# Performance work log

Hardware: AMD Instinct MI355X
Metric: run time of the kernel (lower is better)

The kernel has to match this reference:

```python
import jax, jax.numpy as jnp
import numpy as np

B, C, H, W = 2, 256, 64, 64
NUM_HEADS = 4
DIM_HEAD_QK = 64
DIM_HEAD_V = 64  # dim_out // num_heads
DIM_OUT_QK = NUM_HEADS * DIM_HEAD_QK  # 256
DIM_OUT_V = NUM_HEADS * DIM_HEAD_V    # 256
SCALE = DIM_HEAD_QK ** -0.5


def rel_logits_1d(q, rel_k, permute):
    # q: (Bh, Hq, Wq, d), rel_k: (2*Wq-1, d)
    Bh, Hq, Wq, d = q.shape
    R = 2 * Wq - 1
    x = jnp.einsum('bhwd,rd->bhwr', q, rel_k)              # (Bh, Hq, Wq, R)
    x = x.reshape(-1, Wq, R)
    x_pad = jnp.pad(x, ((0, 0), (0, 0), (0, 1))).reshape(x.shape[0], -1)
    x_pad = jnp.pad(x_pad, ((0, 0), (0, Wq - 1)))
    x_pad = x_pad.reshape(-1, Wq + 1, R)
    x = x_pad[:, :Wq, Wq - 1:]                              # (Bh*Hq, Wq, Wq)
    x = x.reshape(Bh, Hq, 1, Wq, Wq)
    x = jnp.broadcast_to(x, (Bh, Hq, Hq, Wq, Wq))
    return jnp.transpose(x, permute)


def pos_embed_rel(q, height_rel, width_rel):
    # q: (Bh, HW, d)
    Bh = q.shape[0]
    qr = q.reshape(Bh, H, W, -1)
    rel_w = rel_logits_1d(qr, width_rel, (0, 1, 3, 2, 4))   # (Bh, H, W, H, W)
    qt = jnp.transpose(qr, (0, 2, 1, 3))                    # (Bh, W, H, d)
    rel_h = rel_logits_1d(qt, height_rel, (0, 3, 1, 4, 2))  # (Bh, H, W, H, W)
    return (rel_h + rel_w).reshape(Bh, H * W, H * W)


def setup_inputs() -> dict:
    key = jax.random.key(0)
    k1, k2, k3, k4 = jax.random.split(key, 4)
    x = jax.random.normal(k1, (B, C, H, W), dtype=jnp.float32)
    qkv_w = jax.random.normal(k2, (2 * DIM_OUT_QK + DIM_OUT_V, C), dtype=jnp.float32) * (C ** -0.5)
    height_rel = jax.random.normal(k3, (2 * H - 1, DIM_HEAD_QK), dtype=jnp.float32) * SCALE
    width_rel = jax.random.normal(k4, (2 * W - 1, DIM_HEAD_QK), dtype=jnp.float32) * SCALE
    return {"x": x, "qkv_w": qkv_w, "height_rel": height_rel, "width_rel": width_rel}


def reference(x, qkv_w, height_rel, width_rel):
    # 1x1 conv == channel matmul
    qkv = jnp.einsum('bchw,oc->bohw', x, qkv_w)             # (B, 768, H, W)
    q, k, v = jnp.split(qkv, [DIM_OUT_QK, 2 * DIM_OUT_QK], axis=1)
    HW = H * W
    q = q.reshape(B * NUM_HEADS, DIM_HEAD_QK, HW).transpose(0, 2, 1)  # (Bh, HW, d)
    k = k.reshape(B * NUM_HEADS, DIM_HEAD_QK, HW)                     # (Bh, d, HW)
    v = v.reshape(B * NUM_HEADS, DIM_HEAD_V, HW).transpose(0, 2, 1)   # (Bh, HW, dv)
    attn = jnp.einsum('bnd,bdm->bnm', q, k) * SCALE + pos_embed_rel(q, height_rel, width_rel)
    attn = jax.nn.softmax(attn, axis=-1)
    out = jnp.einsum('bnm,bmd->bnd', attn, v)               # (Bh, HW, dv)
    out = out.transpose(0, 2, 1).reshape(B, DIM_OUT_V, H, W)
    return out
```

## Files before the change

### kernel.cpp

```cpp
#include <hip/hip_runtime.h>
#include <hip/hip_bf16.h>

typedef __attribute__((ext_vector_type(8))) short bf16x8;
typedef __attribute__((ext_vector_type(4))) float f32x4;

static __device__ __forceinline__ f32x4 mfma16(bf16x8 a, bf16x8 b, f32x4 c) {
    return __builtin_amdgcn_mfma_f32_16x16x32_bf16(a, b, c, 0, 0, 0);
}

#define LOG2E 1.44269504f

__global__ __launch_bounds__(256, 4) void qkv_kernel(
    const float* __restrict__ x, const float* __restrict__ w,
    __hip_bfloat16* __restrict__ qb, __hip_bfloat16* __restrict__ kb,
    __hip_bfloat16* __restrict__ vt)
{
    alignas(16) __shared__ __hip_bfloat16 sA[64 * 72];
    alignas(16) __shared__ __hip_bfloat16 sB[64 * 72];
    const int nb = blockIdx.x * 64;
    const int ob = blockIdx.y * 64;
    const int b  = blockIdx.z;
    const int tid  = threadIdx.x;
    const int lane = tid & 63;
    const int wv   = tid >> 6;
    const int quad = lane >> 4;
    const int l16  = lane & 15;

    f32x4 acc[4];
    for (int i = 0; i < 4; i++) acc[i] = (f32x4)0.f;

    for (int k0 = 0; k0 < 256; k0 += 64) {
        __syncthreads();
        {
            const int o = tid >> 2, c0 = (tid & 3) << 4;
            const float* srcw = w + (ob + o) * 256 + k0 + c0;
            union { bf16x8 v; __hip_bfloat16 h[8]; } u0, u1;
            #pragma unroll
            for (int i = 0; i < 2; i++) {
                float4 f = *(const float4*)(srcw + i * 4);
                u0.h[4*i+0] = __float2bfloat16(f.x); u0.h[4*i+1] = __float2bfloat16(f.y);
                u0.h[4*i+2] = __float2bfloat16(f.z); u0.h[4*i+3] = __float2bfloat16(f.w);
            }
            #pragma unroll
            for (int i = 0; i < 2; i++) {
                float4 f = *(const float4*)(srcw + 8 + i * 4);
                u1.h[4*i+0] = __float2bfloat16(f.x); u1.h[4*i+1] = __float2bfloat16(f.y);
                u1.h[4*i+2] = __float2bfloat16(f.z); u1.h[4*i+3] = __float2bfloat16(f.w);
            }
            *(bf16x8*)&sA[o * 72 + c0]     = u0.v;
            *(bf16x8*)&sA[o * 72 + c0 + 8] = u1.v;
        }
        {
            const int c = tid >> 2, n0 = (tid & 3) << 4;
            const float* srcx = x + ((size_t)b * 256 + k0 + c) * 4096 + nb + n0;
            #pragma unroll
            for (int i = 0; i < 4; i++) {
                float4 f = *(const float4*)(srcx + i * 4);
                sB[(n0 + 4*i + 0) * 72 + c] = __float2bfloat16(f.x);
                sB[(n0 + 4*i + 1) * 72 + c] = __float2bfloat16(f.y);
                sB[(n0 + 4*i + 2) * 72 + c] = __float2bfloat16(f.z);
                sB[(n0 + 4*i + 3) * 72 + c] = __float2bfloat16(f.w);
            }
        }
        __syncthreads();
        const __hip_bfloat16* aRow = &sA[(16 * wv + l16) * 72];
        #pragma unroll
        for (int ks = 0; ks < 2; ks++) {
            bf16x8 af = *(const bf16x8*)&aRow[ks * 32 + quad * 8];
            #pragma unroll
            for (int ct = 0; ct < 4; ct++) {
                bf16x8 bfv = *(const bf16x8*)&sB[(16 * ct + l16) * 72 + ks * 32 + quad * 8];
                acc[ct] = mfma16(af, bfv, acc[ct]);
            }
        }
    }
    if (ob < 512) {
        #pragma unroll
        for (int ct = 0; ct < 4; ct++) {
            int n = nb + 16 * ct + l16;
            int o0 = ob + 16 * wv + quad * 4;
            union { short4 s; __hip_bfloat16 hh[4]; } u;
            #pragma unroll
            for (int r = 0; r < 4; r++) u.hh[r] = __float2bfloat16(acc[ct][r]);
            int oo = o0 & 255;
            int bhh = b * 4 + (oo >> 6), d = oo & 63;
            __hip_bfloat16* dst = (o0 >= 256 ? kb : qb) + ((size_t)bhh * 4096 + n) * 64 + d;
            *(short4*)dst = u.s;
        }
    } else {
        __syncthreads();
        #pragma unroll
        for (int ct = 0; ct < 4; ct++)
            #pragma unroll
            for (int r = 0; r < 4; r++)
                sA[(16 * wv + quad * 4 + r) * 72 + 16 * ct + l16] = __float2bfloat16(acc[ct][r]);
        int o2 = (ob - 512) + 16 * wv + l16;
        int bhh = b * 4 + (o2 >> 6), d = o2 & 63;
        __hip_bfloat16* dst = vt + ((size_t)bhh * 64 + d) * 4096 + nb + 16 * quad;
        const __hip_bfloat16* srcl = &sA[(16 * wv + l16) * 72 + 16 * quad];
        *(bf16x8*)dst       = *(const bf16x8*)srcl;
        *(bf16x8*)(dst + 8) = *(const bf16x8*)(srcl + 8);
    }
}

__global__ __launch_bounds__(512, 4) void attn_kernel(
    const __hip_bfloat16* __restrict__ qb, const __hip_bfloat16* __restrict__ kb,
    const __hip_bfloat16* __restrict__ vt, const float* __restrict__ hrel,
    const float* __restrict__ wrel, float* __restrict__ out)
{
    alignas(16) __shared__ __hip_bfloat16 sU[18432];
    alignas(16) __shared__ __hip_bfloat16 sRH[64 * 66];

    const int h    = blockIdx.x;
    const int bh   = blockIdx.y;
    const int tid  = threadIdx.x;
    const int lane = tid & 63;
    const int wv   = tid >> 6;
    const int qg   = wv >> 2;
    const int kg   = wv & 3;
    const int quad = lane >> 4;
    const int l16  = lane & 15;

    __hip_bfloat16* sQ   = sU;
    __hip_bfloat16* sW   = sU + 64 * 72;
    __hip_bfloat16* sHRs = sU + 192 * 72;
    __hip_bfloat16* sRWt = sU;
    __hip_bfloat16* sKb  = sU;
    __hip_bfloat16* sVb  = sU + 128 * 72;

    {
        int r = tid >> 3, d8 = (tid & 7) * 8;
        *(bf16x8*)&sQ[r * 72 + d8] =
            *(const bf16x8*)&qb[(((size_t)bh * 4096 + h * 64 + r)) * 64 + d8];
    }
    {
        int r = tid >> 2, c0 = (tid & 3) << 4;
        union { bf16x8 v; __hip_bfloat16 h8[8]; } u0, u1;
        #pragma unroll
        for (int i = 0; i < 2; i++) {
            float4 f = (r < 127) ? *(const float4*)&wrel[r * 64 + c0 + 4*i] : float4{0,0,0,0};
            u0.h8[4*i+0] = __float2bfloat16(f.x); u0.h8[4*i+1] = __float2bfloat16(f.y);
            u0.h8[4*i+2] = __float2bfloat16(f.z); u0.h8[4*i+3] = __float2bfloat16(f.w);
        }
        #pragma unroll
        for (int i = 0; i < 2; i++) {
            float4 f = (r < 127) ? *(const float4*)&wrel[r * 64 + c0 + 8 + 4*i] : float4{0,0,0,0};
            u1.h8[4*i+0] = __float2bfloat16(f.x); u1.h8[4*i+1] = __float2bfloat16(f.y);
            u1.h8[4*i+2] = __float2bfloat16(f.z); u1.h8[4*i+3] = __float2bfloat16(f.w);
        }
        *(bf16x8*)&sW[r * 72 + c0]     = u0.v;
        *(bf16x8*)&sW[r * 72 + c0 + 8] = u1.v;
    }
    {
        int r = tid >> 3, c0 = (tid & 7) * 8;
        union { bf16x8 v; __hip_bfloat16 h8[8]; } u0;
        #pragma unroll
        for (int i = 0; i < 2; i++) {
            float4 f = *(const float4*)&hrel[(63 - h + r) * 64 + c0 + 4*i];
            u0.h8[4*i+0] = __float2bfloat16(f.x); u0.h8[4*i+1] = __float2bfloat16(f.y);
            u0.h8[4*i+2] = __float2bfloat16(f.z); u0.h8[4*i+3] = __float2bfloat16(f.w);
        }
        *(bf16x8*)&sHRs[r * 72 + c0] = u0.v;
    }
    __syncthreads();

    const int g    = wv & 3;
    const int half = wv >> 2;
    const __hip_bfloat16* aRow = &sQ[(16 * g + l16) * 72];
    bf16x8 qf0 = *(const bf16x8*)&aRow[quad * 8];
    bf16x8 qf1 = *(const bf16x8*)&aRow[32 + quad * 8];
    bf16x8 qm[2][2];
    #pragma unroll
    for (int qt = 0; qt < 2; qt++) {
        const __hip_bfloat16* qr = &sQ[(qg * 32 + 16 * qt + l16) * 72];
        qm[qt][0] = *(const bf16x8*)&qr[quad * 8];
        qm[qt][1] = *(const bf16x8*)&qr[32 + quad * 8];
    }
    __syncthreads();

    {
        const int rbase = half * 64;
        #pragma unroll
        for (int ct = 0; ct < 4; ct++) {
            int rr = rbase + 16 * ct + l16;
            f32x4 a = (f32x4)0.f;
            a = mfma16(qf0, *(const bf16x8*)&sW[rr * 72 + quad * 8], a);
            a = mfma16(qf1, *(const bf16x8*)&sW[rr * 72 + 32 + quad * 8], a);
            #pragma unroll
            for (int r = 0; r < 4; r++) {
                int ww = 16 * g + quad * 4 + r;
                int wp = rr + ww - 63;
                if (wp >= 0 && wp < 64) sRWt[ww * 68 + wp] = __float2bfloat16(a[r]);
            }
        }
    }
    if (half == 0) {
        #pragma unroll
        for (int ct = 0; ct < 4; ct++) {
            f32x4 a = (f32x4)0.f;
            a = mfma16(qf0, *(const bf16x8*)&sHRs[(16 * ct + l16) * 72 + quad * 8], a);
            a = mfma16(qf1, *(const bf16x8*)&sHRs[(16 * ct + l16) * 72 + 32 + quad * 8], a);
            #pragma unroll
            for (int r = 0; r < 4; r++)
                sRH[(16 * g + quad * 4 + r) * 66 + 16 * ct + l16] = __float2bfloat16(a[r]);
        }
    }
    __syncthreads();

    union S4 { short4 s; __hip_bfloat16 h[4]; };
    S4 rwp[2][2];
    #pragma unroll
    for (int qt = 0; qt < 2; qt++)
        #pragma unroll
        for (int kt = 0; kt < 2; kt++)
            rwp[qt][kt].s = *(const short4*)&sRWt[(qg * 32 + 16 * qt + l16) * 68
                                                  + 32 * (kg & 1) + 16 * kt + 4 * quad];
    __syncthreads();

    f32x4 oacc[2][4];
    #pragma unroll
    for (int qt = 0; qt < 2; qt++)
        #pragma unroll
        for (int dt = 0; dt < 4; dt++) oacc[qt][dt] = (f32x4)0.f;
    float lsum[2] = {0.f, 0.f};

    const __hip_bfloat16* ksrc = kb + (size_t)bh * 4096 * 64;
    const __hip_bfloat16* vsrc = vt + (size_t)bh * 64 * 4096;

    const int skey = tid >> 2, sd16 = (tid & 3) * 16;
    const int svd  = tid >> 3, sq3  = tid & 7;
    const int skg  = sq3 >> 1, st   = sq3 & 1;
    __hip_bfloat16* stK = &sKb[skey * 72 + sd16];
    __hip_bfloat16* stV = &sVb[svd * 136 + skg * 32 + st * 4];
    const __hip_bfloat16* gK = ksrc + (size_t)skey * 64 + sd16;
    const __hip_bfloat16* gV = vsrc + (size_t)svd * 4096 + sq3 * 16;

    bf16x8 pk0, pk1, pv0, pv1;
    pk0 = *(const bf16x8*)(gK);
    pk1 = *(const bf16x8*)(gK + 8);
    pv0 = *(const bf16x8*)(gV);
    pv1 = *(const bf16x8*)(gV + 8);

    const __hip_bfloat16* kr0  = &sKb[(kg * 32 + l16) * 72 + quad * 8];
    const __hip_bfloat16* vrow = &sVb[l16 * 136 + kg * 32 + quad * 8];
    const __hip_bfloat16* rh0  = &sRH[(qg * 32 + l16) * 66];
    const __hip_bfloat16* rh1  = &sRH[(qg * 32 + 16 + l16) * 66];

    for (int j = 0; j < 32; j++) {
        *(bf16x8*)(stK)     = pk0;
        *(bf16x8*)(stK + 8) = pk1;
        {
            union { bf16x8 v; short4 q[2]; } ua, ub;
            ua.v = pv0; ub.v = pv1;
            *(short4*)(stV)      = ua.q[0];
            *(short4*)(stV + 8)  = ua.q[1];
            *(short4*)(stV + 16) = ub.q[0];
            *(short4*)(stV + 24) = ub.q[1];
        }
        __syncthreads();
        if (j < 31) {
            size_t kb0 = (size_t)(j + 1) * 128;
            pk0 = *(const bf16x8*)(gK + kb0 * 64);
            pk1 = *(const bf16x8*)(gK + kb0 * 64 + 8);
            pv0 = *(const bf16x8*)(gV + kb0);
            pv1 = *(const bf16x8*)(gV + kb0 + 8);
        }

        bf16x8 kf00 = *(const bf16x8*)(kr0);
        bf16x8 kf01 = *(const bf16x8*)(kr0 + 32);
        bf16x8 kf10 = *(const bf16x8*)(kr0 + 16 * 72);
        bf16x8 kf11 = *(const bf16x8*)(kr0 + 16 * 72 + 32);

        const int hp = 2 * j + (kg >> 1);
        bf16x8 pa[2];
        #pragma unroll
        for (int qt = 0; qt < 2; qt++) {
            f32x4 s0 = (f32x4)0.f, s1 = (f32x4)0.f;
            s0 = mfma16(kf00, qm[qt][0], s0);
            s0 = mfma16(kf01, qm[qt][1], s0);
            s1 = mfma16(kf10, qm[qt][0], s1);
            s1 = mfma16(kf11, qm[qt][1], s1);
            float rhb = LOG2E * __bfloat162float((qt ? rh1 : rh0)[hp]);
            union { bf16x8 v; __hip_bfloat16 hh[8]; } pu;
            #pragma unroll
            for (int r = 0; r < 4; r++) {
                float p = __builtin_amdgcn_exp2f(
                    fmaf(s0[r], 0.125f * LOG2E,
                         fmaf(__bfloat162float(rwp[qt][0].h[r]), LOG2E, rhb)));
                lsum[qt] += p;
                pu.hh[r] = __float2bfloat16(p);
            }
            #pragma unroll
            for (int r = 0; r < 4; r++) {
                float p = __builtin_amdgcn_exp2f(
                    fmaf(s1[r], 0.125f * LOG2E,
                         fmaf(__bfloat162float(rwp[qt][1].h[r]), LOG2E, rhb)));
                lsum[qt] += p;
                pu.hh[4 + r] = __float2bfloat16(p);
            }
            pa[qt] = pu.v;
        }

        #pragma unroll
        for (int dt = 0; dt < 4; dt++) {
            bf16x8 vf = *(const bf16x8*)(vrow + dt * 16 * 136);
            oacc[0][dt] = mfma16(pa[0], vf, oacc[0][dt]);
            oacc[1][dt] = mfma16(pa[1], vf, oacc[1][dt]);
        }
        __syncthreads();
    }

    #pragma unroll
    for (int qt = 0; qt < 2; qt++) {
        lsum[qt] += __shfl_xor(lsum[qt], 16, 64);
        lsum[qt] += __shfl_xor(lsum[qt], 32, 64);
    }

    float* obuf  = (float*)sU;
    float* slbuf = obuf + 4608;
    for (int rnd = 1; rnd < 4; rnd++) {
        if (kg == rnd) {
            #pragma unroll
            for (int qt = 0; qt < 2; qt++)
                #pragma unroll
                for (int dt = 0; dt < 4; dt++)
                    *(f32x4*)&obuf[qg * 2304 + (16 * dt + l16) * 36 + 16 * qt + 4 * quad]
                        = oacc[qt][dt];
            if (quad == 0) {
                slbuf[qg * 64 + l16]      = lsum[0];
                slbuf[qg * 64 + 16 + l16] = lsum[1];
            }
        }
        __syncthreads();
        if (kg == 0) {
            #pragma unroll
            for (int qt = 0; qt < 2; qt++)
                #pragma unroll
                for (int dt = 0; dt < 4; dt++)
                    oacc[qt][dt] += *(const f32x4*)&obuf[qg * 2304 + (16 * dt + l16) * 36
                                                          + 16 * qt + 4 * quad];
            lsum[0] += slbuf[qg * 64 + l16];
            lsum[1] += slbuf[qg * 64 + 16 + l16];
        }
        __syncthreads();
    }

    if (kg == 0) {
        if (quad == 0) {
            slbuf[qg * 64 + l16]      = lsum[0];
            slbuf[qg * 64 + 16 + l16] = lsum[1];
        }
        const int b = bh >> 2, head = bh & 3;
        #pragma unroll
        for (int qt = 0; qt < 2; qt++) {
            f32x4 lv;
            #pragma unroll
            for (int r = 0; r < 4; r++)
                lv[r] = 1.f / slbuf[qg * 64 + 16 * qt + 4 * quad + r];
            #pragma unroll
            for (int dt = 0; dt < 4; dt++) {
                f32x4 o = oacc[qt][dt] * lv;
                int dv = 16 * dt + l16;
                int q0 = qg * 32 + 16 * qt + 4 * quad;
                *(f32x4*)&out[((size_t)(b * 256 + head * 64 + dv)) * 4096 + h * 64 + q0] = o;
            }
        }
    }
}

extern "C" void kernel_launch(void* const* d_in, const int* in_sizes, int n_in,
                              void* d_out, int out_size, void* d_ws, size_t ws_size,
                              hipStream_t stream) {
    const float* x     = (const float*)d_in[0];
    const float* qkv_w = (const float*)d_in[1];
    const float* hrel  = (const float*)d_in[2];
    const float* wrel  = (const float*)d_in[3];
    float* out = (float*)d_out;

    __hip_bfloat16* qb = (__hip_bfloat16*)d_ws;
    __hip_bfloat16* kb = qb + (size_t)8 * 4096 * 64;
    __hip_bfloat16* vt = kb + (size_t)8 * 4096 * 64;

    qkv_kernel<<<dim3(64, 12, 2), 256, 0, stream>>>(x, qkv_w, qb, kb, vt);
    attn_kernel<<<dim3(64, 8), 512, 0, stream>>>(qb, kb, vt, hrel, wrel, out);
}
```

Before: 138.7 us.

## Double-buffer K/V tiles via direct global-to-LDS loads with XOR-swizzled layouts

The attention kernel now streams K and V tiles straight into LDS with global_load_lds into two 32KB buffers, prefetching the next tile while the current one is computed. The register-staged copy and one barrier per iteration go away. The QKV kernel writes K and V^T in an XOR-swizzled global layout so the 16-byte direct LDS loads land bank-conflict-free, and the sB staging in the QKV GEMM is swizzled too. Dynamic shared memory grows to 64KB per block, which may lower occupancy, and correctness depends on swizzle consistency and on the single remaining barrier per iteration guarding buffer reuse.

New measurement: 131.5 us. -5.2%, faster.

```diff
diff --git a/kernel.cpp b/kernel.cpp
--- a/kernel.cpp
+++ b/kernel.cpp
@@ -6,6 +6,11 @@
 
 static __device__ __forceinline__ f32x4 mfma16(bf16x8 a, bf16x8 b, f32x4 c) {
     return __builtin_amdgcn_mfma_f32_16x16x32_bf16(a, b, c, 0, 0, 0);
+}
+static __device__ __forceinline__ void gll16(const void* g, void* l) {
+    __builtin_amdgcn_global_load_lds(
+        (const __attribute__((address_space(1))) unsigned int*)g,
+        (__attribute__((address_space(3))) unsigned int*)l, 16, 0, 0);
 }
 
 #define LOG2E 1.44269504f
@@ -52,14 +57,15 @@
         }
         {
             const int c = tid >> 2, n0 = (tid & 3) << 4;
+            const int csw = c ^ ((tid & 3) * 16);
             const float* srcx = x + ((size_t)b * 256 + k0 + c) * 4096 + nb + n0;
             #pragma unroll
             for (int i = 0; i < 4; i++) {
                 float4 f = *(const float4*)(srcx + i * 4);
-                sB[(n0 + 4*i + 0) * 72 + c] = __float2bfloat16(f.x);
-                sB[(n0 + 4*i + 1) * 72 + c] = __float2bfloat16(f.y);
-                sB[(n0 + 4*i + 2) * 72 + c] = __float2bfloat16(f.z);
-                sB[(n0 + 4*i + 3) * 72 + c] = __float2bfloat16(f.w);
+                sB[(n0 + 4*i + 0) * 72 + csw] = __float2bfloat16(f.x);
+                sB[(n0 + 4*i + 1) * 72 + csw] = __float2bfloat16(f.y);
+                sB[(n0 + 4*i + 2) * 72 + csw] = __float2bfloat16(f.z);
+                sB[(n0 + 4*i + 3) * 72 + csw] = __float2bfloat16(f.w);
             }
         }
         __syncthreads();
@@ -69,7 +75,8 @@
             bf16x8 af = *(const bf16x8*)&aRow[ks * 32 + quad * 8];
             #pragma unroll
             for (int ct = 0; ct < 4; ct++) {
-                bf16x8 bfv = *(const bf16x8*)&sB[(16 * ct + l16) * 72 + ks * 32 + quad * 8];
+                bf16x8 bfv = *(const bf16x8*)&sB[(16 * ct + l16) * 72
+                                                 + ((ks * 32 + quad * 8) ^ (ct * 16))];
                 acc[ct] = mfma16(af, bfv, acc[ct]);
             }
         }
@@ -84,8 +91,11 @@
             for (int r = 0; r < 4; r++) u.hh[r] = __float2bfloat16(acc[ct][r]);
             int oo = o0 & 255;
             int bhh = b * 4 + (oo >> 6), d = oo & 63;
-            __hip_bfloat16* dst = (o0 >= 256 ? kb : qb) + ((size_t)bhh * 4096 + n) * 64 + d;
-            *(short4*)dst = u.s;
+            if (o0 < 256) {
+                *(short4*)(qb + ((size_t)bhh * 4096 + n) * 64 + d) = u.s;
+            } else {
+                *(short4*)(kb + ((size_t)bhh * 4096 + n) * 64 + (d ^ ((n & 7) << 3))) = u.s;
+            }
         }
     } else {
         __syncthreads();
@@ -96,10 +106,17 @@
                 sA[(16 * wv + quad * 4 + r) * 72 + 16 * ct + l16] = __float2bfloat16(acc[ct][r]);
         int o2 = (ob - 512) + 16 * wv + l16;
         int bhh = b * 4 + (o2 >> 6), d = o2 & 63;
-        __hip_bfloat16* dst = vt + ((size_t)bhh * 64 + d) * 4096 + nb + 16 * quad;
         const __hip_bfloat16* srcl = &sA[(16 * wv + l16) * 72 + 16 * quad];
-        *(bf16x8*)dst       = *(const bf16x8*)srcl;
-        *(bf16x8*)(dst + 8) = *(const bf16x8*)(srcl + 8);
+        __hip_bfloat16* vrow = vt + ((size_t)bhh * 64 + d) * 4096;
+        const int kt = quad & 1;
+        const int gbase = nb + (quad >> 1) * 32;
+        const int dsw = (d & 7) << 3;
+        #pragma unroll
+        for (int m = 0; m < 4; m++) {
+            short4 val = *(const short4*)(srcl + 4 * m);
+            int P4 = gbase + 8 * m + 4 * kt;
+            *(short4*)(vrow + (P4 ^ dsw)) = val;
+        }
     }
 }
 
@@ -108,7 +125,7 @@
     const __hip_bfloat16* __restrict__ vt, const float* __restrict__ hrel,
     const float* __restrict__ wrel, float* __restrict__ out)
 {
-    alignas(16) __shared__ __hip_bfloat16 sU[18432];
+    extern __shared__ __align__(16) char smem[];
     alignas(16) __shared__ __hip_bfloat16 sRH[64 * 66];
 
     const int h    = blockIdx.x;
@@ -121,12 +138,10 @@
     const int quad = lane >> 4;
     const int l16  = lane & 15;
 
-    __hip_bfloat16* sQ   = sU;
-    __hip_bfloat16* sW   = sU + 64 * 72;
-    __hip_bfloat16* sHRs = sU + 192 * 72;
-    __hip_bfloat16* sRWt = sU;
-    __hip_bfloat16* sKb  = sU;
-    __hip_bfloat16* sVb  = sU + 128 * 72;
+    __hip_bfloat16* sQ   = (__hip_bfloat16*)smem;
+    __hip_bfloat16* sW   = (__hip_bfloat16*)smem + 64 * 72;
+    __hip_bfloat16* sHRs = (__hip_bfloat16*)smem + 192 * 72;
+    __hip_bfloat16* sRWt = (__hip_bfloat16*)smem;
 
     {
         int r = tid >> 3, d8 = (tid & 7) * 8;
@@ -217,6 +232,16 @@
                                                   + 32 * (kg & 1) + 16 * kt + 4 * quad];
     __syncthreads();
 
+    const char* kT = (const char*)kb + (size_t)bh * 524288 + wv * 1024 + lane * 16;
+    const char* vT = (const char*)vt + (size_t)bh * 524288
+                     + (size_t)(wv * 4 + quad) * 8192 + l16 * 16;
+
+    gll16(kT,           smem + wv * 1024);
+    gll16(kT + 8192,    smem + 8192 + wv * 1024);
+    gll16(vT,           smem + 16384 + wv * 1024);
+    gll16(vT + 262144,  smem + 24576 + wv * 1024);
+    __syncthreads();
+
     f32x4 oacc[2][4];
     #pragma unroll
     for (int qt = 0; qt < 2; qt++)
@@ -224,52 +249,32 @@
         for (int dt = 0; dt < 4; dt++) oacc[qt][dt] = (f32x4)0.f;
     float lsum[2] = {0.f, 0.f};
 
-    const __hip_bfloat16* ksrc = kb + (size_t)bh * 4096 * 64;
-    const __hip_bfloat16* vsrc = vt + (size_t)bh * 64 * 4096;
-
-    const int skey = tid >> 2, sd16 = (tid & 3) * 16;
-    const int svd  = tid >> 3, sq3  = tid & 7;
-    const int skg  = sq3 >> 1, st   = sq3 & 1;
-    __hip_bfloat16* stK = &sKb[skey * 72 + sd16];
-    __hip_bfloat16* stV = &sVb[svd * 136 + skg * 32 + st * 4];
-    const __hip_bfloat16* gK = ksrc + (size_t)skey * 64 + sd16;
-    const __hip_bfloat16* gV = vsrc + (size_t)svd * 4096 + sq3 * 16;
-
-    bf16x8 pk0, pk1, pv0, pv1;
-    pk0 = *(const bf16x8*)(gK);
-    pk1 = *(const bf16x8*)(gK + 8);
-    pv0 = *(const bf16x8*)(gV);
-    pv1 = *(const bf16x8*)(gV + 8);
-
-    const __hip_bfloat16* kr0  = &sKb[(kg * 32 + l16) * 72 + quad * 8];
-    const __hip_bfloat16* vrow = &sVb[l16 * 136 + kg * 32 + quad * 8];
-    const __hip_bfloat16* rh0  = &sRH[(qg * 32 + l16) * 66];
-    const __hip_bfloat16* rh1  = &sRH[(qg * 32 + 16 + l16) * 66];
+    const int krowOff = (kg * 32 + l16) * 128;
+    const int sw  = (l16 & 7) << 4;
+    const int kA  = (quad * 16) ^ sw;
+    const int kB  = (64 + quad * 16) ^ sw;
+    const int vOff = 16384 + l16 * 256 + ((kg * 64 + quad * 16) ^ sw);
+
+    const __hip_bfloat16* rh0 = &sRH[(qg * 32 + l16) * 66];
+    const __hip_bfloat16* rh1 = &sRH[(qg * 32 + 16 + l16) * 66];
 
     for (int j = 0; j < 32; j++) {
-        *(bf16x8*)(stK)     = pk0;
-        *(bf16x8*)(stK + 8) = pk1;
-        {
-            union { bf16x8 v; short4 q[2]; } ua, ub;
-            ua.v = pv0; ub.v = pv1;
-            *(short4*)(stV)      = ua.q[0];
-            *(short4*)(stV + 8)  = ua.q[1];
-            *(short4*)(stV + 16) = ub.q[0];
-            *(short4*)(stV + 24) = ub.q[1];
-        }
-        __syncthreads();
+        const char* buf = smem + (j & 1) * 32768;
         if (j < 31) {
-            size_t kb0 = (size_t)(j + 1) * 128;
-            pk0 = *(const bf16x8*)(gK + kb0 * 64);
-            pk1 = *(const bf16x8*)(gK + kb0 * 64 + 8);
-            pv0 = *(const bf16x8*)(gV + kb0);
-            pv1 = *(const bf16x8*)(gV + kb0 + 8);
-        }
-
-        bf16x8 kf00 = *(const bf16x8*)(kr0);
-        bf16x8 kf01 = *(const bf16x8*)(kr0 + 32);
-        bf16x8 kf10 = *(const bf16x8*)(kr0 + 16 * 72);
-        bf16x8 kf11 = *(const bf16x8*)(kr0 + 16 * 72 + 32);
+            char* nbuf = smem + ((j + 1) & 1) * 32768;
+            const char* gk = kT + (size_t)(j + 1) * 16384;
+            gll16(gk,          nbuf + wv * 1024);
+            gll16(gk + 8192,   nbuf + 8192 + wv * 1024);
+            const char* gv = vT + (size_t)(j + 1) * 256;
+            gll16(gv,          nbuf + 16384 + wv * 1024);
+            gll16(gv + 262144, nbuf + 24576 + wv * 1024);
+        }
+
+        const char* kr = buf + krowOff;
+        bf16x8 kf00 = *(const bf16x8*)(kr + kA);
+        bf16x8 kf01 = *(const bf16x8*)(kr + kB);
+        bf16x8 kf10 = *(const bf16x8*)(kr + 2048 + kA);
+        bf16x8 kf11 = *(const bf16x8*)(kr + 2048 + kB);
 
         const int hp = 2 * j + (kg >> 1);
         bf16x8 pa[2];
@@ -303,7 +308,7 @@
 
         #pragma unroll
         for (int dt = 0; dt < 4; dt++) {
-            bf16x8 vf = *(const bf16x8*)(vrow + dt * 16 * 136);
+            bf16x8 vf = *(const bf16x8*)(buf + vOff + dt * 4096);
             oacc[0][dt] = mfma16(pa[0], vf, oacc[0][dt]);
             oacc[1][dt] = mfma16(pa[1], vf, oacc[1][dt]);
         }
@@ -316,7 +321,7 @@
         lsum[qt] += __shfl_xor(lsum[qt], 32, 64);
     }
 
-    float* obuf  = (float*)sU;
+    float* obuf  = (float*)smem;
     float* slbuf = obuf + 4608;
     for (int rnd = 1; rnd < 4; rnd++) {
         if (kg == rnd) {
@@ -382,5 +387,5 @@
     __hip_bfloat16* vt = kb + (size_t)8 * 4096 * 64;
 
     qkv_kernel<<<dim3(64, 12, 2), 256, 0, stream>>>(x, qkv_w, qb, kb, vt);
-    attn_kernel<<<dim3(64, 8), 512, 0, stream>>>(qb, kb, vt, hrel, wrel, out);
-}
+    attn_kernel<<<dim3(64, 8), 512, 65536, stream>>>(qb, kb, vt, hrel, wrel, out);
+}
```
